# Optimization experiments

Hardware: AMD Instinct MI355X
Metric: run time of the kernel (lower is better)

The kernel has to match this reference:

```python
import jax, jax.numpy as jnp
import numpy as np

N_NODES = 4000
N_EDGES = 4000
D_IN = 20      # data_length
HID = 768      # hidden_dim
OUT = 2        # output_dim


def _lin(k, i, o):
    s = 1.0 / np.sqrt(i)
    return jax.random.uniform(k, (i, o), jnp.float32, -s, s)


def setup_inputs() -> dict:
    key = jax.random.key(0)
    ks = jax.random.split(key, 16)
    T = N_NODES + N_EDGES
    data = jax.random.normal(ks[0], (N_NODES, D_IN), jnp.float32)
    data_mask = jnp.ones((N_NODES,), jnp.float32)  # unused by forward, kept for signature fidelity
    e_adj_matrix = jax.random.uniform(ks[1], (T, T), jnp.float32) * (2.0 / T)
    transition = jax.random.randint(ks[2], (2, N_EDGES), 0, N_NODES)
    # exactly N_EDGES ones interleaved among N_NODES zeros
    inx = jnp.concatenate([jnp.ones((N_EDGES,), jnp.int32), jnp.zeros((N_NODES,), jnp.int32)])
    label_inx_positive = jax.random.permutation(ks[3], inx)
    label_inx = jax.random.randint(ks[4], (T,), 0, OUT)
    mask = jax.random.randint(ks[5], (T,), 0, 2).astype(jnp.float32)
    return {
        'data': data, 'data_mask': data_mask, 'e_adj_matrix': e_adj_matrix,
        'transition': transition, 'label_inx_positive': label_inx_positive,
        'label_inx': label_inx, 'mask': mask,
        'mlp_w1': _lin(ks[6], 6 * D_IN, HID), 'mlp_b1': jnp.zeros((HID,), jnp.float32),
        'mlp_w2': _lin(ks[7], HID, HID), 'mlp_b2': jnp.zeros((HID,), jnp.float32),
        'mlp2_w1': _lin(ks[8], D_IN, HID), 'mlp2_b1': jnp.zeros((HID,), jnp.float32),
        'mlp2_w2': _lin(ks[9], HID, HID), 'mlp2_b2': jnp.zeros((HID,), jnp.float32),
        'gcn_w1': _lin(ks[10], HID, HID), 'gcn_b1': jnp.zeros((HID,), jnp.float32),
        'gcn_w2': _lin(ks[11], HID, OUT), 'gcn_b2': jnp.zeros((OUT,), jnp.float32),
    }


def gen_edge2(x, trans):
    # Vectorized Gen_edge2: e1 = [x[t1], x[t0]]; e2 = [x[t0], x[t1]] iff reverse edge exists; e3 = e1 + e2.
    t0, t1 = trans[0], trans[1]
    n = x.shape[0]
    keys = t0 * n + t1
    rkeys = t1 * n + t0
    sk = jnp.sort(keys)
    pos = jnp.clip(jnp.searchsorted(sk, rkeys), 0, sk.shape[0] - 1)
    has_rev = sk[pos] == rkeys  # [E]
    e1 = jnp.concatenate([x[t1], x[t0]], axis=1)  # [E, 2d]
    e2 = jnp.where(has_rev[:, None], jnp.concatenate([x[t0], x[t1]], axis=1), 0.0)
    return jnp.concatenate([e1, e2, e1 + e2], axis=1)  # [E, 6d]


def dataset_cgraph(n_feat, e_feat, e_inx):
    # Vectorized interleave: pull next edge row where e_inx==1, else next node row.
    m = e_inx == 1
    idx_e = jnp.clip(jnp.cumsum(m.astype(jnp.int32)) - 1, 0, e_feat.shape[0] - 1)
    idx_n = jnp.clip(jnp.cumsum((~m).astype(jnp.int32)) - 1, 0, n_feat.shape[0] - 1)
    return jnp.where(m[:, None], e_feat[idx_e], n_feat[idx_n])  # [N+E, H]


def reference(data, data_mask, e_adj_matrix, transition, label_inx_positive,
              label_inx, mask, mlp_w1, mlp_b1, mlp_w2, mlp_b2,
              mlp2_w1, mlp2_b1, mlp2_w2, mlp2_b2,
              gcn_w1, gcn_b1, gcn_w2, gcn_b2):
    e_feat = gen_edge2(data, transition)                              # [E, 120]
    e_feat = jax.nn.relu(e_feat @ mlp_w1 + mlp_b1) @ mlp_w2 + mlp_b2  # [E, H]
    n_feat = jax.nn.relu(data @ mlp2_w1 + mlp2_b1) @ mlp2_w2 + mlp2_b2  # [N, H]
    x = dataset_cgraph(n_feat, e_feat, label_inx_positive)            # [N+E, H]
    # 2-layer GCN (GcnModel assumed standard: relu(A X W1), then A H W2)
    h1 = jax.nn.relu(e_adj_matrix @ (x @ gcn_w1) + gcn_b1)            # [N+E, H]
    logits = e_adj_matrix @ (h1 @ gcn_w2) + gcn_b2                    # [N+E, OUT]
    logp = jax.nn.log_softmax(logits, axis=-1)
    ce = -jnp.take_along_axis(logp, label_inx[:, None], axis=1)[:, 0]
    loss = jnp.sum(ce * mask) / jnp.maximum(jnp.sum(mask), 1.0)
    return logits, loss, h1
```

## Files before the change

kernel.cpp:

```cpp
#include <hip/hip_runtime.h>
#include <hip/hip_bf16.h>

#define N_NODES 4000
#define N_EDGES 4000
#define T_ALL   8000
#define HID     768

typedef __attribute__((ext_vector_type(8))) short bf16x8;
typedef __attribute__((ext_vector_type(4))) short s16x4;
typedef __attribute__((ext_vector_type(4))) float f32x4;

__device__ __forceinline__ short f2bf(float f) {
    union { float f; unsigned u; } a; a.f = f;
    unsigned u = a.u;
    unsigned r = (u + 0x7fffu + ((u >> 16) & 1u)) >> 16;
    return (short)(r & 0xffffu);
}
__device__ __forceinline__ float bf2f(short s) {
    union { unsigned u; float f; } a;
    a.u = ((unsigned)(unsigned short)s) << 16;
    return a.f;
}
__device__ __forceinline__ void gload_lds16(const void* g, void* l) {
    __builtin_amdgcn_global_load_lds(
        (const __attribute__((address_space(1))) void*)g,
        (__attribute__((address_space(3))) void*)l, 16, 0, 0);
}

__global__ __launch_bounds__(512, 2) void gemm_ring(
    const short* __restrict__ A, const short* __restrict__ BT,
    short* __restrict__ parts, int M, int K, int lda, int ldbt)
{
    __shared__ __align__(16) short As[4][256 * 32];
    __shared__ __align__(16) short Bs[4][256 * 32];
    const int t    = threadIdx.x;
    const int lane = t & 63;
    const int wv   = t >> 6;
    const int wm   = wv >> 2;
    const int wn   = wv & 3;
    const int lrow = lane & 15;
    const int kgrp = lane >> 4;

    const int nwg  = gridDim.x * gridDim.y * gridDim.z;
    int flat = blockIdx.x + gridDim.x * (blockIdx.y + gridDim.y * blockIdx.z);
    int w    = (flat & 7) * (nwg >> 3) + (flat >> 3);
    const int bx = w % 3;
    int rest = w / 3;
    const int by = rest & 31;
    const int bz = rest >> 5;
    const int bm0 = by << 8;
    const int bn0 = bx << 8;

    const int TC = K >> 5;
    const int Z  = gridDim.z;
    const int q  = TC / Z, r = TC % Z;
    const int nt   = q + (bz < r ? 1 : 0);
    const int kbeg = ((bz < r) ? bz * (q + 1) : r * (q + 1) + (bz - r) * q) << 5;

    auto stageA = [&](int tt) {
        const int k0 = kbeg + (tt << 5);
        short* dst = &As[tt & 3][0];
#pragma unroll
        for (int i = 0; i < 2; ++i) {
            int f = t + (i << 9);
            int row = f >> 2, sl = f & 3;
            int ga = bm0 + row; ga = ga < M ? ga : M - 1;
            gload_lds16(A + (size_t)ga * lda + k0 + ((sl ^ ((row >> 1) & 3)) << 3),
                        dst + f * 8);
        }
    };
    auto stageB = [&](int tt) {
        const int k0 = kbeg + (tt << 5);
        short* dst = &Bs[tt & 3][0];
#pragma unroll
        for (int i = 0; i < 2; ++i) {
            int f = t + (i << 9);
            int row = f >> 2, sl = f & 3;
            gload_lds16(BT + (size_t)(bn0 + row) * ldbt + k0 + ((sl ^ ((row >> 1) & 3)) << 3),
                        dst + f * 8);
        }
    };

    f32x4 acc[8][4];
#pragma unroll
    for (int m = 0; m < 8; ++m)
#pragma unroll
        for (int n = 0; n < 4; ++n) acc[m][n] = (f32x4)(0.0f);

    stageA(0); stageB(0);
    stageA(1); stageB(1);
    stageA(2); stageB(2);
    asm volatile("s_waitcnt vmcnt(4)" ::: "memory");
    __builtin_amdgcn_s_barrier();

    bf16x8 r0A0[4], r0A1[4], r0B[4];
    bf16x8 r1A0[4], r1A1[4], r1B[4];

    {
        const short* Ac = &As[0][0];
        const short* Bc = &Bs[0][0];
#pragma unroll
        for (int m = 0; m < 4; ++m) {
            int rr = (wm << 7) + (m << 4) + lrow;
            r0A0[m] = *reinterpret_cast<const bf16x8*>(
                &Ac[(rr << 5) + ((kgrp ^ ((rr >> 1) & 3)) << 3)]);
        }
#pragma unroll
        for (int n = 0; n < 4; ++n) {
            int rr = (wn << 6) + (n << 4) + lrow;
            r0B[n] = *reinterpret_cast<const bf16x8*>(
                &Bc[(rr << 5) + ((kgrp ^ ((rr >> 1) & 3)) << 3)]);
        }
#pragma unroll
        for (int m = 0; m < 4; ++m) {
            int rr = (wm << 7) + 64 + (m << 4) + lrow;
            r0A1[m] = *reinterpret_cast<const bf16x8*>(
                &Ac[(rr << 5) + ((kgrp ^ ((rr >> 1) & 3)) << 3)]);
        }
    }

#define TILE_STEP(TT, cA0, cA1, cB, nA0, nA1, nB)                              \
    {                                                                          \
        const int _tt = (TT);                                                  \
        if (_tt + 1 < nt) {                                                    \
            const short* An = &As[(_tt + 1) & 3][0];                           \
            const short* Bn = &Bs[(_tt + 1) & 3][0];                           \
            _Pragma("unroll")                                                  \
            for (int m = 0; m < 4; ++m) {                                      \
                int rr = (wm << 7) + (m << 4) + lrow;                          \
                nA0[m] = *reinterpret_cast<const bf16x8*>(                     \
                    &An[(rr << 5) + ((kgrp ^ ((rr >> 1) & 3)) << 3)]);         \
            }                                                                  \
            _Pragma("unroll")                                                  \
            for (int n = 0; n < 4; ++n) {                                      \
                int rr = (wn << 6) + (n << 4) + lrow;                          \
                nB[n] = *reinterpret_cast<const bf16x8*>(                      \
                    &Bn[(rr << 5) + ((kgrp ^ ((rr >> 1) & 3)) << 3)]);         \
            }                                                                  \
            _Pragma("unroll")                                                  \
            for (int m = 0; m < 4; ++m) {                                      \
                int rr = (wm << 7) + 64 + (m << 4) + lrow;                     \
                nA1[m] = *reinterpret_cast<const bf16x8*>(                     \
                    &An[(rr << 5) + ((kgrp ^ ((rr >> 1) & 3)) << 3)]);         \
            }                                                                  \
        }                                                                      \
        if (_tt + 3 < nt) { stageA(_tt + 3); stageB(_tt + 3); }                \
        __builtin_amdgcn_sched_barrier(0);                                     \
        __builtin_amdgcn_s_setprio(1);                                         \
        _Pragma("unroll")                                                      \
        for (int m = 0; m < 4; ++m)                                            \
            _Pragma("unroll")                                                  \
            for (int n = 0; n < 4; ++n)                                        \
                acc[m][n] = __builtin_amdgcn_mfma_f32_16x16x32_bf16(           \
                    cA0[m], cB[n], acc[m][n], 0, 0, 0);                        \
        _Pragma("unroll")                                                      \
        for (int m = 0; m < 4; ++m)                                            \
            _Pragma("unroll")                                                  \
            for (int n = 0; n < 4; ++n)                                        \
                acc[4 + m][n] = __builtin_amdgcn_mfma_f32_16x16x32_bf16(       \
                    cA1[m], cB[n], acc[4 + m][n], 0, 0, 0);                    \
        __builtin_amdgcn_s_setprio(0);                                         \
        if (_tt <= nt - 4) asm volatile("s_waitcnt vmcnt(4)" ::: "memory");    \
        else               asm volatile("s_waitcnt vmcnt(0)" ::: "memory");    \
        __builtin_amdgcn_s_barrier();                                          \
    }

    int tt = 0;
    for (; tt + 1 < nt; tt += 2) {
        TILE_STEP(tt,     r0A0, r0A1, r0B, r1A0, r1A1, r1B);
        TILE_STEP(tt + 1, r1A0, r1A1, r1B, r0A0, r0A1, r0B);
    }
    if (tt < nt) TILE_STEP(tt, r0A0, r0A1, r0B, r1A0, r1A1, r1B);
#undef TILE_STEP

    short* Cp = parts + (size_t)bz * 6144000;
#pragma unroll
    for (int m = 0; m < 8; ++m) {
        int r0 = bm0 + (wm << 7) + (m << 4) + (kgrp << 2);
#pragma unroll
        for (int n = 0; n < 4; ++n) {
            int col = bn0 + (wn << 6) + (n << 4) + lrow;
#pragma unroll
            for (int j = 0; j < 4; ++j) {
                int rr = r0 + j;
                if (rr < M) Cp[(size_t)rr * 768 + col] = f2bf(acc[m][n][j]);
            }
        }
    }
}

template<int BIAS, int RELU, int OUTBF, int AF32>
__global__ __launch_bounds__(256) void gemm_bf(
    const void* __restrict__ Av, const short* __restrict__ BT,
    const float* __restrict__ bias, void* __restrict__ Cv,
    int M, int N, int K, int lda, int ldbt, int ldc)
{
    __shared__ __align__(16) short As[2][128 * 64];
    __shared__ __align__(16) short Bs[2][128 * 64];
    const int t    = threadIdx.x;
    const int lane = t & 63;
    const int wave = t >> 6;
    const int wr   = (wave >> 1) << 6;
    const int wc   = (wave & 1) << 6;
    const int lrow = lane & 15;
    const int kgrp = lane >> 4;
    const int bm0  = blockIdx.y << 7;
    const int bn0  = blockIdx.x << 7;
    const short* Ab = (const short*)Av;
    const float* Af = (const float*)Av;

    const int nk = K >> 6;

    auto stage = [&](int kt, int buf) {
        const int k0 = kt << 6;
#pragma unroll
        for (int i = 0; i < 4; ++i) {
            int f = t + (i << 8);
            int row = f >> 3, slot = f & 7;
            int gb = bn0 + row; gb = (gb < N) ? gb : (N - 1);
            gload_lds16(BT + (size_t)gb * ldbt + k0 + ((slot ^ (row & 7)) << 3),
                        &Bs[buf][((i << 8) + (wave << 6)) * 8]);
        }
        if constexpr (!AF32) {
#pragma unroll
            for (int i = 0; i < 4; ++i) {
                int f = t + (i << 8);
                int row = f >> 3, slot = f & 7;
                int ga = bm0 + row; ga = (ga < M) ? ga : (M - 1);
                gload_lds16(Ab + (size_t)ga * lda + k0 + ((slot ^ (row & 7)) << 3),
                            &As[buf][((i << 8) + (wave << 6)) * 8]);
            }
        } else {
#pragma unroll
            for (int i = 0; i < 4; ++i) {
                int f = t + (i << 8);
                int row = f >> 3, c8 = f & 7;
                int ga = bm0 + row; ga = (ga < M) ? ga : (M - 1);
                const float* ap = Af + (size_t)ga * lda + k0 + (c8 << 3);
                float4 v0 = *reinterpret_cast<const float4*>(ap);
                float4 v1 = *reinterpret_cast<const float4*>(ap + 4);
                union { bf16x8 v; short s[8]; } u;
                u.s[0] = f2bf(v0.x); u.s[1] = f2bf(v0.y); u.s[2] = f2bf(v0.z); u.s[3] = f2bf(v0.w);
                u.s[4] = f2bf(v1.x); u.s[5] = f2bf(v1.y); u.s[6] = f2bf(v1.z); u.s[7] = f2bf(v1.w);
                *reinterpret_cast<bf16x8*>(&As[buf][row * 64 + ((c8 ^ (row & 7)) << 3)]) = u.v;
            }
        }
    };

    f32x4 acc[4][4];
#pragma unroll
    for (int m = 0; m < 4; ++m)
#pragma unroll
        for (int n = 0; n < 4; ++n) acc[m][n] = (f32x4)(0.0f);

    auto compute = [&](int buf) {
#pragma unroll
        for (int kk = 0; kk < 2; ++kk) {
            bf16x8 af[4], bfv[4];
#pragma unroll
            for (int m = 0; m < 4; ++m) {
                int rr = wr + m * 16 + lrow;
                af[m] = *reinterpret_cast<const bf16x8*>(
                    &As[buf][rr * 64 + (((kk * 4 + kgrp) ^ (rr & 7)) << 3)]);
            }
#pragma unroll
            for (int n = 0; n < 4; ++n) {
                int rr = wc + n * 16 + lrow;
                bfv[n] = *reinterpret_cast<const bf16x8*>(
                    &Bs[buf][rr * 64 + (((kk * 4 + kgrp) ^ (rr & 7)) << 3)]);
            }
#pragma unroll
            for (int m = 0; m < 4; ++m)
#pragma unroll
                for (int n = 0; n < 4; ++n)
                    acc[m][n] = __builtin_amdgcn_mfma_f32_16x16x32_bf16(
                        af[m], bfv[n], acc[m][n], 0, 0, 0);
        }
    };

    if constexpr (!AF32) {
        stage(0, 0);
        if (nk > 1) stage(1, 1);
        for (int kt = 0; kt < nk - 1; ++kt) {
            asm volatile("s_waitcnt vmcnt(8)" ::: "memory");
            __builtin_amdgcn_s_barrier();
            compute(kt & 1);
            __builtin_amdgcn_s_barrier();
            if (kt + 2 < nk) stage(kt + 2, kt & 1);
        }
        asm volatile("s_waitcnt vmcnt(0)" ::: "memory");
        __builtin_amdgcn_s_barrier();
        compute((nk - 1) & 1);
    } else {
        stage(0, 0);
        __syncthreads();
        int cur = 0;
        for (int kt = 0; kt < nk; ++kt) {
            if (kt + 1 < nk) stage(kt + 1, cur ^ 1);
            compute(cur);
            __syncthreads();
            cur ^= 1;
        }
    }

    short* Cb = (short*)Cv;
    float* Cf = (float*)Cv;
#pragma unroll
    for (int m = 0; m < 4; ++m) {
        int rbase = bm0 + wr + m * 16 + kgrp * 4;
#pragma unroll
        for (int n = 0; n < 4; ++n) {
            int col = bn0 + wc + n * 16 + lrow;
            if (col >= N) continue;
            float bv = BIAS ? bias[col] : 0.0f;
#pragma unroll
            for (int j = 0; j < 4; ++j) {
                int rr = rbase + j;
                if (rr < M) {
                    float v = acc[m][n][j] + bv;
                    if (RELU) v = fmaxf(v, 0.0f);
                    if (OUTBF) Cb[(size_t)rr * ldc + col] = f2bf(v);
                    else       Cf[(size_t)rr * ldc + col] = v;
                }
            }
        }
    }
}

template<int RELU>
__global__ __launch_bounds__(256) void gemm_sel(
    const short* __restrict__ A,
    const short* __restrict__ BT1, const short* __restrict__ BT2,
    const float* __restrict__ bias1, const float* __restrict__ bias2,
    short* __restrict__ C, int K)
{
    __shared__ __align__(16) short As[2][128 * 64];
    __shared__ __align__(16) short Bs[2][128 * 64];
    const int t    = threadIdx.x;
    const int lane = t & 63;
    const int wave = t >> 6;
    const int wr   = (wave >> 1) << 6;
    const int wc   = (wave & 1) << 6;
    const int lrow = lane & 15;
    const int kgrp = lane >> 4;
    const int bm0  = blockIdx.y << 7;
    const int bn0  = blockIdx.x << 7;
    const short* BT   = (bm0 < 4096) ? BT1 : BT2;
    const float* bias = (bm0 < 4096) ? bias1 : bias2;
    const int nk = K >> 6;

    auto stage = [&](int kt, int buf) {
        const int k0 = kt << 6;
#pragma unroll
        for (int i = 0; i < 4; ++i) {
            int f = t + (i << 8);
            int row = f >> 3, slot = f & 7;
            gload_lds16(BT + (size_t)(bn0 + row) * K + k0 + ((slot ^ (row & 7)) << 3),
                        &Bs[buf][((i << 8) + (wave << 6)) * 8]);
        }
#pragma unroll
        for (int i = 0; i < 4; ++i) {
            int f = t + (i << 8);
            int row = f >> 3, slot = f & 7;
            gload_lds16(A + (size_t)(bm0 + row) * K + k0 + ((slot ^ (row & 7)) << 3),
                        &As[buf][((i << 8) + (wave << 6)) * 8]);
        }
    };

    f32x4 acc[4][4];
#pragma unroll
    for (int m = 0; m < 4; ++m)
#pragma unroll
        for (int n = 0; n < 4; ++n) acc[m][n] = (f32x4)(0.0f);

    auto compute = [&](int buf) {
#pragma unroll
        for (int kk = 0; kk < 2; ++kk) {
            bf16x8 af[4], bfv[4];
#pragma unroll
            for (int m = 0; m < 4; ++m) {
                int rr = wr + m * 16 + lrow;
                af[m] = *reinterpret_cast<const bf16x8*>(
                    &As[buf][rr * 64 + (((kk * 4 + kgrp) ^ (rr & 7)) << 3)]);
            }
#pragma unroll
            for (int n = 0; n < 4; ++n) {
                int rr = wc + n * 16 + lrow;
                bfv[n] = *reinterpret_cast<const bf16x8*>(
                    &Bs[buf][rr * 64 + (((kk * 4 + kgrp) ^ (rr & 7)) << 3)]);
            }
#pragma unroll
            for (int m = 0; m < 4; ++m)
#pragma unroll
                for (int n = 0; n < 4; ++n)
                    acc[m][n] = __builtin_amdgcn_mfma_f32_16x16x32_bf16(
                        af[m], bfv[n], acc[m][n], 0, 0, 0);
        }
    };

    stage(0, 0);
    if (nk > 1) stage(1, 1);
    for (int kt = 0; kt < nk - 1; ++kt) {
        asm volatile("s_waitcnt vmcnt(8)" ::: "memory");
        __builtin_amdgcn_s_barrier();
        compute(kt & 1);
        __builtin_amdgcn_s_barrier();
        if (kt + 2 < nk) stage(kt + 2, kt & 1);
    }
    asm volatile("s_waitcnt vmcnt(0)" ::: "memory");
    __builtin_amdgcn_s_barrier();
    compute((nk - 1) & 1);

#pragma unroll
    for (int m = 0; m < 4; ++m) {
        int rbase = bm0 + wr + m * 16 + kgrp * 4;
#pragma unroll
        for (int n = 0; n < 4; ++n) {
            int col = bn0 + wc + n * 16 + lrow;
            float bv = bias[col];
#pragma unroll
            for (int j = 0; j < 4; ++j) {
                float v = acc[m][n][j] + bv;
                if (RELU) v = fmaxf(v, 0.0f);
                C[(size_t)(rbase + j) * 768 + col] = f2bf(v);
            }
        }
    }
}

__global__ __launch_bounds__(256) void prep_all(
    const float* __restrict__ data, const int* __restrict__ trans,
    const float* __restrict__ w1, const float* __restrict__ w2,
    const float* __restrict__ w21, const float* __restrict__ w22,
    const float* __restrict__ gw1, const int* __restrict__ einx,
    short* __restrict__ w1T, short* __restrict__ w2T,
    short* __restrict__ w21T, short* __restrict__ w22T,
    short* __restrict__ gw1T, short* __restrict__ estack,
    int* __restrict__ src)
{
    __shared__ float tile[32][33];
    __shared__ int ibuf[512];
    const int blk = blockIdx.x, tid = threadIdx.x;

    if (blk < 2496) {
        if (blk < 384) {
            int i = blk * 256 + tid, n = i >> 7, k = i & 127;
            w1T[i] = (k < 120) ? f2bf(w1[k * 768 + n]) : (short)0;
        } else if (blk < 1344) {
            if (blk < 960) {
                int j = blk - 384, bx = j % 24, by = j / 24;
                int c0 = bx << 5, r0 = by << 5, tx = tid & 31, ty = tid >> 5;
#pragma unroll
                for (int i = ty; i < 32; i += 8)
                    tile[i][tx] = w2[(size_t)(r0 + i) * 768 + c0 + tx];
                __syncthreads();
#pragma unroll
                for (int i = ty; i < 32; i += 8)
                    w2T[(size_t)(c0 + i) * 768 + r0 + tx] = f2bf(tile[tx][i]);
            } else {
                int i = (blk - 960) * 256 + tid, n = i >> 7, k = i & 127;
                w21T[i] = (k < 20) ? f2bf(w21[k * 768 + n]) : (short)0;
            }
        } else if (blk < 1920) {
            int j = blk - 1344, bx = j % 24, by = j / 24;
            int c0 = bx << 5, r0 = by << 5, tx = tid & 31, ty = tid >> 5;
#pragma unroll
            for (int i = ty; i < 32; i += 8)
                tile[i][tx] = w22[(size_t)(r0 + i) * 768 + c0 + tx];
            __syncthreads();
#pragma unroll
            for (int i = ty; i < 32; i += 8)
                w22T[(size_t)(c0 + i) * 768 + r0 + tx] = f2bf(tile[tx][i]);
        } else {
            int j = blk - 1920, bx = j % 24, by = j / 24;
            int c0 = bx << 5, r0 = by << 5, tx = tid & 31, ty = tid >> 5;
#pragma unroll
            for (int i = ty; i < 32; i += 8)
                tile[i][tx] = gw1[(size_t)(r0 + i) * 768 + c0 + tx];
            __syncthreads();
#pragma unroll
            for (int i = ty; i < 32; i += 8)
                gw1T[(size_t)(c0 + i) * 768 + r0 + tx] = f2bf(tile[tx][i]);
        }
    } else if (blk < 6496) {
        int e = blk - 2496;
        int t0 = trans[e], t1 = trans[N_EDGES + e];
        __shared__ int found;
        if (tid == 0) found = 0;
        __syncthreads();
        for (int j = tid; j < N_EDGES; j += 256)
            if (trans[j] == t1 && trans[N_EDGES + j] == t0) found = 1;
        __syncthreads();
        float h = found ? 1.0f : 0.0f;
        short* rp = estack + (size_t)e * 128;
        if (tid < 20) {
            float x0 = data[t0 * 20 + tid];
            float x1 = data[t1 * 20 + tid];
            rp[tid]        = f2bf(x1);
            rp[20 + tid]   = f2bf(x0);
            rp[40 + tid]   = f2bf(h * x0);
            rp[60 + tid]   = f2bf(h * x1);
            rp[80 + tid]   = f2bf(x1 + h * x0);
            rp[100 + tid]  = f2bf(x0 + h * x1);
        } else if (tid < 28) {
            rp[120 + (tid - 20)] = 0;
        }
    } else if (blk < 8496) {
        int i = (blk - 6496) * 256 + tid;
        int r = i >> 7, c = i & 127;
        estack[(size_t)(4096) * 128 + i] = (c < 20) ? f2bf(data[r * 20 + c]) : (short)0;
    } else {
        int* partial = ibuf;
        int* excl    = ibuf + 256;
        int base = tid * 32;
        int cnt = 0;
        for (int i = 0; i < 32; ++i) {
            int idx = base + i;
            if (idx < T_ALL) cnt += (einx[idx] == 1);
        }
        partial[tid] = cnt;
        __syncthreads();
        if (tid == 0) {
            int s = 0;
            for (int i = 0; i < 256; ++i) { excl[i] = s; s += partial[i]; }
        }
        __syncthreads();
        int ce = excl[tid];
        int cn = base - ce;
        for (int i = 0; i < 32; ++i) {
            int idx = base + i;
            if (idx >= T_ALL) break;
            if (einx[idx] == 1) { src[idx] = N_NODES + ce; ce++; }
            else                { src[idx] = cn; cn++; }
        }
    }
}

__global__ __launch_bounds__(192) void reduce_h1_hw(
    const short* __restrict__ p, const float* __restrict__ bias,
    const float* __restrict__ w2, float* __restrict__ h1, float* __restrict__ hw,
    int Z)
{
    int r = blockIdx.x, t = threadIdx.x;
    int c0 = t * 4;
    size_t base = (size_t)r * 768 + c0;
    float a[4];
#pragma unroll
    for (int j = 0; j < 4; ++j) a[j] = bias[c0 + j];
    for (int z = 0; z < Z; ++z) {
        s16x4 v = *reinterpret_cast<const s16x4*>(p + (size_t)z * 6144000 + base);
#pragma unroll
        for (int j = 0; j < 4; ++j) a[j] += bf2f(v[j]);
    }
    float d0 = 0.0f, d1 = 0.0f;
    float4 o;
#pragma unroll
    for (int j = 0; j < 4; ++j) {
        float v = fmaxf(a[j], 0.0f);
        ((float*)&o)[j] = v;
        d0 += v * w2[(c0 + j) * 2];
        d1 += v * w2[(c0 + j) * 2 + 1];
    }
    *reinterpret_cast<float4*>(h1 + base) = o;
#pragma unroll
    for (int off = 32; off > 0; off >>= 1) {
        d0 += __shfl_down(d0, off);
        d1 += __shfl_down(d1, off);
    }
    __shared__ float s0[3], s1[3];
    int wvv = t >> 6, ln = t & 63;
    if (ln == 0) { s0[wvv] = d0; s1[wvv] = d1; }
    __syncthreads();
    if (t == 0) {
        hw[r * 2]     = s0[0] + s0[1] + s0[2];
        hw[r * 2 + 1] = s1[0] + s1[1] + s1[2];
    }
}


__global__ void cvt_bf16(const float* __restrict__ in, short* __restrict__ out, int n8)
{
    int i = blockIdx.x * 256 + threadIdx.x;
    if (i >= n8) return;
    float4 v0 = *reinterpret_cast<const float4*>(in + (size_t)i * 8);
    float4 v1 = *reinterpret_cast<const float4*>(in + (size_t)i * 8 + 4);
    union { bf16x8 v; short s[8]; } u;
    u.s[0] = f2bf(v0.x); u.s[1] = f2bf(v0.y); u.s[2] = f2bf(v0.z); u.s[3] = f2bf(v0.w);
    u.s[4] = f2bf(v1.x); u.s[5] = f2bf(v1.y); u.s[6] = f2bf(v1.z); u.s[7] = f2bf(v1.w);
    *reinterpret_cast<bf16x8*>(out + (size_t)i * 8) = u.v;
}

__global__ void gather_x(const short* __restrict__ nfeat, const short* __restrict__ efeat,
                         const int* __restrict__ src, short* __restrict__ x)
{
    int i = blockIdx.x * 256 + threadIdx.x;
    int r = i / 96, c = i % 96;
    int s = src[r];
    const bf16x8* rowp = (s >= N_NODES)
        ? reinterpret_cast<const bf16x8*>(efeat + (size_t)(s - N_NODES) * HID)
        : reinterpret_cast<const bf16x8*>(nfeat + (size_t)s * HID);
    reinterpret_cast<bf16x8*>(x)[i] = rowp[c];
}

__global__ void h1w2_kernel(const float* __restrict__ h1, const float* __restrict__ w2,
                            float* __restrict__ hw)
{
    int wave = threadIdx.x >> 6, lane = threadIdx.x & 63;
    int row = blockIdx.x * 4 + wave;
    const float* hp = h1 + (size_t)row * HID;
    float a0 = 0.0f, a1 = 0.0f;
    for (int k = lane; k < HID; k += 64) {
        float h = hp[k];
        a0 += h * w2[k * 2];
        a1 += h * w2[k * 2 + 1];
    }
    for (int off = 32; off > 0; off >>= 1) {
        a0 += __shfl_down(a0, off);
        a1 += __shfl_down(a1, off);
    }
    if (lane == 0) { hw[row * 2] = a0; hw[row * 2 + 1] = a1; }
}

__global__ __launch_bounds__(256) void adj_hw_bf(const short* __restrict__ A,
    const float* __restrict__ hw, const float* __restrict__ b2, float* __restrict__ logits)
{
    int row = blockIdx.x;
    const short* ar = A + (size_t)row * T_ALL;
    float a0 = 0.0f, a1 = 0.0f;
    for (int c = threadIdx.x; c < 1000; c += 256) {
        bf16x8 v = *reinterpret_cast<const bf16x8*>(ar + c * 8);
#pragma unroll
        for (int j = 0; j < 8; ++j) {
            float av = bf2f(v[j]);
            int k = c * 8 + j;
            a0 += av * hw[k * 2];
            a1 += av * hw[k * 2 + 1];
        }
    }
    __shared__ float s0[256], s1[256];
    s0[threadIdx.x] = a0; s1[threadIdx.x] = a1;
    __syncthreads();
    for (int o = 128; o > 0; o >>= 1) {
        if (threadIdx.x < o) {
            s0[threadIdx.x] += s0[threadIdx.x + o];
            s1[threadIdx.x] += s1[threadIdx.x + o];
        }
        __syncthreads();
    }
    if (threadIdx.x == 0) {
        logits[row * 2]     = s0[0] + b2[0];
        logits[row * 2 + 1] = s1[0] + b2[1];
    }
}

__global__ __launch_bounds__(256) void adj_hw_f32(const float* __restrict__ A,
    const float* __restrict__ hw, const float* __restrict__ b2, float* __restrict__ logits)
{
    int row = blockIdx.x;
    const float* ar = A + (size_t)row * T_ALL;
    float a0 = 0.0f, a1 = 0.0f;
    for (int k = threadIdx.x; k < T_ALL; k += 256) {
        float v = ar[k];
        a0 += v * hw[k * 2];
        a1 += v * hw[k * 2 + 1];
    }
    __shared__ float s0[256], s1[256];
    s0[threadIdx.x] = a0; s1[threadIdx.x] = a1;
    __syncthreads();
    for (int o = 128; o > 0; o >>= 1) {
        if (threadIdx.x < o) {
            s0[threadIdx.x] += s0[threadIdx.x + o];
            s1[threadIdx.x] += s1[threadIdx.x + o];
        }
        __syncthreads();
    }
    if (threadIdx.x == 0) {
        logits[row * 2]     = s0[0] + b2[0];
        logits[row * 2 + 1] = s1[0] + b2[1];
    }
}

__global__ __launch_bounds__(256) void loss_kernel(const float* __restrict__ logits,
    const int* __restrict__ label, const float* __restrict__ mask, float* __restrict__ outp)
{
    __shared__ float sc[256], sm[256];
    float ac = 0.0f, am = 0.0f;
    for (int i = threadIdx.x; i < T_ALL; i += 256) {
        float l0 = logits[i * 2], l1 = logits[i * 2 + 1];
        float mx = fmaxf(l0, l1);
        float lse = mx + logf(expf(l0 - mx) + expf(l1 - mx));
        float li = label[i] ? l1 : l0;
        ac += (lse - li) * mask[i];
        am += mask[i];
    }
    sc[threadIdx.x] = ac; sm[threadIdx.x] = am;
    __syncthreads();
    for (int o = 128; o > 0; o >>= 1) {
        if (threadIdx.x < o) {
            sc[threadIdx.x] += sc[threadIdx.x + o];
            sm[threadIdx.x] += sm[threadIdx.x + o];
        }
        __syncthreads();
    }
    if (threadIdx.x == 0) *outp = sc[0] / fmaxf(sm[0], 1.0f);
}


extern "C" void kernel_launch(void* const* d_in, const int* in_sizes, int n_in,
                              void* d_out, int out_size, void* d_ws, size_t ws_size,
                              hipStream_t stream)
{
    (void)in_sizes; (void)n_in; (void)out_size;

    const float* data  = (const float*)d_in[0];
    const float* adj   = (const float*)d_in[2];
    const int*   trans = (const int*)d_in[3];
    const int*   einx  = (const int*)d_in[4];
    const int*   label = (const int*)d_in[5];
    const float* mask  = (const float*)d_in[6];
    const float* w1    = (const float*)d_in[7];
    const float* b1    = (const float*)d_in[8];
    const float* w2    = (const float*)d_in[9];
    const float* b2    = (const float*)d_in[10];
    const float* w21   = (const float*)d_in[11];
    const float* b21   = (const float*)d_in[12];
    const float* w22   = (const float*)d_in[13];
    const float* b22   = (const float*)d_in[14];
    const float* gw1   = (const float*)d_in[15];
    const float* gb1   = (const float*)d_in[16];
    const float* gw2   = (const float*)d_in[17];
    const float* gb2   = (const float*)d_in[18];

    char* W = (char*)d_ws;
    short* w1T    = (short*)(W + 0);
    short* w2T    = (short*)(W + 196608);
    short* w21T   = (short*)(W + 1376256);
    short* w22T   = (short*)(W + 1572864);
    short* gw1T   = (short*)(W + 2752512);
    short* estack = (short*)(W + 3932160);
    short* C1s    = (short*)(W + 6029312);
    short* F2s    = (short*)(W + 18612224);
    short* xbuf   = (short*)(W + 31195136);
    int*   src    = (int*)(W + 43499136);

    const bool mid  = (ws_size >= (size_t)140352000);
    const bool big2 = (ws_size >= (size_t)189504000);
    const bool big3 = (ws_size >= (size_t)238656000);
    short* adjbf = (short*)W;
    short* xwT;  float* hwbuf;  short* parts = nullptr;
    if (mid) {
        xwT   = (short*)(W + 128000000);
        hwbuf = (float*)(W + 140288000);
        if (big2) parts = (short*)(W + 140352000);
    } else {
        xwT   = (short*)(W + 48425856);
        hwbuf = (float*)(W + 60713856);
    }

    float* out    = (float*)d_out;
    float* logits = out;
    float* lossp  = out + 16000;
    float* h1     = out + 16001;

    prep_all<<<8497, 256, 0, stream>>>(data, trans, w1, w2, w21, w22, gw1, einx,
                                       w1T, w2T, w21T, w22T, gw1T, estack, src);

    gemm_sel<1><<<dim3(6, 64), 256, 0, stream>>>(estack, w1T, w21T, b1, b21, C1s, 128);
    gemm_sel<0><<<dim3(6, 64), 256, 0, stream>>>(C1s, w2T, w22T, b2, b22, F2s, 768);

    gather_x<<<3000, 256, 0, stream>>>(F2s + (size_t)4096 * 768, F2s, src, xbuf);

    gemm_bf<0, 0, 1, 0><<<dim3(63, 6), 256, 0, stream>>>(gw1T, xbuf, nullptr, xwT, 768, 8000, 768, 768, 768, 8000);

    if (mid) {
        cvt_bf16<<<31250, 256, 0, stream>>>(adj, adjbf, 8000000);
        if (big2) {
            const int Z = big3 ? 8 : 4;
            gemm_ring<<<dim3(3, 32, Z), 512, 0, stream>>>(adjbf, xwT, parts, 8000, 8000, 8000, 8000);
            reduce_h1_hw<<<8000, 192, 0, stream>>>(parts, gb1, gw2, h1, hwbuf, Z);
        } else {
            gemm_bf<1, 1, 0, 0><<<dim3(6, 63), 256, 0, stream>>>(adjbf, xwT, gb1, h1, 8000, 768, 8000, 8000, 8000, 768);
            h1w2_kernel<<<2000, 256, 0, stream>>>(h1, gw2, hwbuf);
        }
        adj_hw_bf<<<8000, 256, 0, stream>>>(adjbf, hwbuf, gb2, logits);
    } else {
        gemm_bf<1, 1, 0, 1><<<dim3(6, 63), 256, 0, stream>>>(adj, xwT, gb1, h1, 8000, 768, 8000, 8000, 8000, 768);
        h1w2_kernel<<<2000, 256, 0, stream>>>(h1, gw2, hwbuf);
        adj_hw_f32<<<8000, 256, 0, stream>>>(adj, hwbuf, gb2, logits);
    }
    loss_kernel<<<1, 256, 0, stream>>>(logits, label, mask, lossp);
}
```

Measured before the change: 325.3 us.

## Overlap fp32-to-bf16 adjacency conversion with early prep and GEMM kernels

Splits the 8000x8000 adjacency fp32-to-bf16 conversion into 2048-element chunks and hands them to extra blocks appended to prep_all, both gemm_sel launches and the xW GEMM. The small early kernels leave most CUs idle, so the bandwidth-bound conversion can fill them instead of running as its own serial kernel. The big-workspace path is given a new buffer layout so the bf16 adjacency does not overlap buffers still in use. Extra blocks may contend for bandwidth with the GEMM blocks, and the offsets must be exactly right to avoid clobbering live data.

```diff
diff --git a/kernel.cpp b/kernel.cpp
--- a/kernel.cpp
+++ b/kernel.cpp
@@ -25,6 +25,18 @@
     __builtin_amdgcn_global_load_lds(
         (const __attribute__((address_space(1))) void*)g,
         (__attribute__((address_space(3))) void*)l, 16, 0, 0);
+}
+
+__device__ __forceinline__ void cvt_job(const float* __restrict__ src,
+                                        short* __restrict__ dst, int chunk)
+{
+    size_t i = (size_t)chunk * 2048 + threadIdx.x * 8;
+    float4 v0 = *reinterpret_cast<const float4*>(src + i);
+    float4 v1 = *reinterpret_cast<const float4*>(src + i + 4);
+    union { bf16x8 v; short s[8]; } u;
+    u.s[0] = f2bf(v0.x); u.s[1] = f2bf(v0.y); u.s[2] = f2bf(v0.z); u.s[3] = f2bf(v0.w);
+    u.s[4] = f2bf(v1.x); u.s[5] = f2bf(v1.y); u.s[6] = f2bf(v1.z); u.s[7] = f2bf(v1.w);
+    *reinterpret_cast<bf16x8*>(dst + i) = u.v;
 }
 
 __global__ __launch_bounds__(512, 2) void gemm_ring(
@@ -193,10 +205,17 @@
 __global__ __launch_bounds__(256) void gemm_bf(
     const void* __restrict__ Av, const short* __restrict__ BT,
     const float* __restrict__ bias, void* __restrict__ Cv,
-    int M, int N, int K, int lda, int ldbt, int ldc)
+    int M, int N, int K, int lda, int ldbt, int ldc,
+    const float* __restrict__ cvsrc, short* __restrict__ cvdst,
+    int cvoff, int cvcnt, int xsplit)
 {
     __shared__ __align__(16) short As[2][128 * 64];
     __shared__ __align__(16) short Bs[2][128 * 64];
+    if ((int)blockIdx.x >= xsplit) {
+        int jid = ((int)blockIdx.x - xsplit) + ((int)gridDim.x - xsplit) * (int)blockIdx.y;
+        if (jid < cvcnt) cvt_job(cvsrc, cvdst, jid + cvoff);
+        return;
+    }
     const int t    = threadIdx.x;
     const int lane = t & 63;
     const int wave = t >> 6;
@@ -332,10 +351,17 @@
     const short* __restrict__ A,
     const short* __restrict__ BT1, const short* __restrict__ BT2,
     const float* __restrict__ bias1, const float* __restrict__ bias2,
-    short* __restrict__ C, int K)
+    short* __restrict__ C, int K,
+    const float* __restrict__ cvsrc, short* __restrict__ cvdst,
+    int cvoff, int cvcnt, int xsplit)
 {
     __shared__ __align__(16) short As[2][128 * 64];
     __shared__ __align__(16) short Bs[2][128 * 64];
+    if ((int)blockIdx.x >= xsplit) {
+        int jid = ((int)blockIdx.x - xsplit) + ((int)gridDim.x - xsplit) * (int)blockIdx.y;
+        if (jid < cvcnt) cvt_job(cvsrc, cvdst, jid + cvoff);
+        return;
+    }
     const int t    = threadIdx.x;
     const int lane = t & 63;
     const int wave = t >> 6;
@@ -436,11 +462,19 @@
     short* __restrict__ w1T, short* __restrict__ w2T,
     short* __restrict__ w21T, short* __restrict__ w22T,
     short* __restrict__ gw1T, short* __restrict__ estack,
-    int* __restrict__ src)
+    int* __restrict__ src,
+    const float* __restrict__ cvsrc, short* __restrict__ cvdst,
+    int cvoff, int cvcnt)
 {
     __shared__ float tile[32][33];
     __shared__ int ibuf[512];
     const int blk = blockIdx.x, tid = threadIdx.x;
+
+    if (blk >= 8497) {
+        int jid = blk - 8497;
+        if (jid < cvcnt) cvt_job(cvsrc, cvdst, jid + cvoff);
+        return;
+    }
 
     if (blk < 2496) {
         if (blk < 384) {
@@ -741,11 +775,41 @@
     short* C1s    = (short*)(W + 6029312);
     short* F2s    = (short*)(W + 18612224);
     short* xbuf   = (short*)(W + 31195136);
-    int*   src    = (int*)(W + 43499136);
+    int*   src    = (int*)(W + 43483136);
 
     const bool mid  = (ws_size >= (size_t)140352000);
     const bool big2 = (ws_size >= (size_t)189504000);
     const bool big3 = (ws_size >= (size_t)238656000);
+
+    float* out    = (float*)d_out;
+    float* logits = out;
+    float* lossp  = out + 16000;
+    float* h1     = out + 16001;
+
+    if (big3) {
+        short* parts = (short*)(W + 0);
+        short* xwT   = (short*)(W + 98304000);
+        float* hwbuf = (float*)(W + 110592000);
+        short* adjbf = (short*)(W + 110656000);
+
+        prep_all<<<8497 + 7813, 256, 0, stream>>>(data, trans, w1, w2, w21, w22, gw1, einx,
+                                                  w1T, w2T, w21T, w22T, gw1T, estack, src,
+                                                  adj, adjbf, 0, 7813);
+        gemm_sel<1><<<dim3(6 + 123, 64), 256, 0, stream>>>(estack, w1T, w21T, b1, b21, C1s, 128,
+                                                           adj, adjbf, 7813, 7813, 6);
+        gemm_sel<0><<<dim3(6 + 123, 64), 256, 0, stream>>>(C1s, w2T, w22T, b2, b22, F2s, 768,
+                                                           adj, adjbf, 15626, 7812, 6);
+        gather_x<<<3000, 256, 0, stream>>>(F2s + (size_t)4096 * 768, F2s, src, xbuf);
+        gemm_bf<0, 0, 1, 0><<<dim3(63 + 1302, 6), 256, 0, stream>>>(
+            gw1T, xbuf, nullptr, xwT, 768, 8000, 768, 768, 768, 8000,
+            adj, adjbf, 23438, 7812, 63);
+        gemm_ring<<<dim3(3, 32, 8), 512, 0, stream>>>(adjbf, xwT, parts, 8000, 8000, 8000, 8000);
+        reduce_h1_hw<<<8000, 192, 0, stream>>>(parts, gb1, gw2, h1, hwbuf, 8);
+        adj_hw_bf<<<8000, 256, 0, stream>>>(adjbf, hwbuf, gb2, logits);
+        loss_kernel<<<1, 256, 0, stream>>>(logits, label, mask, lossp);
+        return;
+    }
+
     short* adjbf = (short*)W;
     short* xwT;  float* hwbuf;  short* parts = nullptr;
     if (mid) {
@@ -757,34 +821,31 @@
         hwbuf = (float*)(W + 60713856);
     }
 
-    float* out    = (float*)d_out;
-    float* logits = out;
-    float* lossp  = out + 16000;
-    float* h1     = out + 16001;
-
     prep_all<<<8497, 256, 0, stream>>>(data, trans, w1, w2, w21, w22, gw1, einx,
-                                       w1T, w2T, w21T, w22T, gw1T, estack, src);
-
-    gemm_sel<1><<<dim3(6, 64), 256, 0, stream>>>(estack, w1T, w21T, b1, b21, C1s, 128);
-    gemm_sel<0><<<dim3(6, 64), 256, 0, stream>>>(C1s, w2T, w22T, b2, b22, F2s, 768);
-
+                                       w1T, w2T, w21T, w22T, gw1T, estack, src,
+                                       nullptr, nullptr, 0, 0);
+    gemm_sel<1><<<dim3(6, 64), 256, 0, stream>>>(estack, w1T, w21T, b1, b21, C1s, 128,
+                                                 nullptr, nullptr, 0, 0, 1 << 30);
+    gemm_sel<0><<<dim3(6, 64), 256, 0, stream>>>(C1s, w2T, w22T, b2, b22, F2s, 768,
+                                                 nullptr, nullptr, 0, 0, 1 << 30);
     gather_x<<<3000, 256, 0, stream>>>(F2s + (size_t)4096 * 768, F2s, src, xbuf);
-
-    gemm_bf<0, 0, 1, 0><<<dim3(63, 6), 256, 0, stream>>>(gw1T, xbuf, nullptr, xwT, 768, 8000, 768, 768, 768, 8000);
+    gemm_bf<0, 0, 1, 0><<<dim3(63, 6), 256, 0, stream>>>(gw1T, xbuf, nullptr, xwT,
+        768, 8000, 768, 768, 768, 8000, nullptr, nullptr, 0, 0, 1 << 30);
 
     if (mid) {
         cvt_bf16<<<31250, 256, 0, stream>>>(adj, adjbf, 8000000);
         if (big2) {
-            const int Z = big3 ? 8 : 4;
-            gemm_ring<<<dim3(3, 32, Z), 512, 0, stream>>>(adjbf, xwT, parts, 8000, 8000, 8000, 8000);
-            reduce_h1_hw<<<8000, 192, 0, stream>>>(parts, gb1, gw2, h1, hwbuf, Z);
+            gemm_ring<<<dim3(3, 32, 4), 512, 0, stream>>>(adjbf, xwT, parts, 8000, 8000, 8000, 8000);
+            reduce_h1_hw<<<8000, 192, 0, stream>>>(parts, gb1, gw2, h1, hwbuf, 4);
         } else {
-            gemm_bf<1, 1, 0, 0><<<dim3(6, 63), 256, 0, stream>>>(adjbf, xwT, gb1, h1, 8000, 768, 8000, 8000, 8000, 768);
+            gemm_bf<1, 1, 0, 0><<<dim3(6, 63), 256, 0, stream>>>(adjbf, xwT, gb1, h1,
+                8000, 768, 8000, 8000, 8000, 768, nullptr, nullptr, 0, 0, 1 << 30);
             h1w2_kernel<<<2000, 256, 0, stream>>>(h1, gw2, hwbuf);
         }
         adj_hw_bf<<<8000, 256, 0, stream>>>(adjbf, hwbuf, gb2, logits);
     } else {
-        gemm_bf<1, 1, 0, 1><<<dim3(6, 63), 256, 0, stream>>>(adj, xwT, gb1, h1, 8000, 768, 8000, 8000, 8000, 768);
+        gemm_bf<1, 1, 0, 1><<<dim3(6, 63), 256, 0, stream>>>(adj, xwT, gb1, h1,
+            8000, 768, 8000, 8000, 8000, 768, nullptr, nullptr, 0, 0, 1 << 30);
         h1w2_kernel<<<2000, 256, 0, stream>>>(h1, gw2, hwbuf);
         adj_hw_f32<<<8000, 256, 0, stream>>>(adj, hwbuf, gb2, logits);
     }
```

Result: slower. 338.7 us (+4.1%).
